# Performance work log

Hardware: AMD Instinct MI355X
Metric: run time of the kernel (lower is better)

The kernel has to match this reference:

```python
import jax, jax.numpy as jnp
import numpy as np

H = 1024
V = 50257
S = 4096

def setup_inputs() -> dict:
    key = jax.random.key(0)
    ks = jax.random.split(key, 16)
    s = 0.02
    return {
        "word_input": jax.random.randint(ks[0], (1,), 0, V),
        "h0": jax.random.normal(ks[1], (1, 1, H), jnp.float32),
        "c0": jax.random.normal(ks[2], (1, 1, H), jnp.float32),
        "encoder_outputs": jax.random.normal(ks[3], (S, 1, H), jnp.float32),
        "embedding": jax.random.normal(ks[4], (V, H), jnp.float32) * s,
        "W_ih": jax.random.normal(ks[5], (4 * H, H), jnp.float32) * s,
        "W_hh": jax.random.normal(ks[6], (4 * H, H), jnp.float32) * s,
        "b_ih": jnp.zeros((4 * H,), jnp.float32),
        "b_hh": jnp.zeros((4 * H,), jnp.float32),
        "attn_W": jax.random.normal(ks[7], (H, H), jnp.float32) * s,
        "attn_b": jnp.zeros((H,), jnp.float32),
        "out_W": jax.random.normal(ks[8], (V, 2 * H), jnp.float32) * s,
        "out_b": jnp.zeros((V,), jnp.float32),
    }


def reference(word_input, h0, c0, encoder_outputs, embedding, W_ih, W_hh,
              b_ih, b_hh, attn_W, attn_b, out_W, out_b):
    # Embedding lookup: (1, H)
    x = embedding[word_input]
    h_prev = h0[0]  # (1, H)
    c_prev = c0[0]  # (1, H)
    # Single-step single-layer LSTM (PyTorch gate order i, f, g, o)
    gates = x @ W_ih.T + b_ih + h_prev @ W_hh.T + b_hh  # (1, 4H)
    i_g, f_g, g_g, o_g = jnp.split(gates, 4, axis=1)
    c_new = jax.nn.sigmoid(f_g) * c_prev + jax.nn.sigmoid(i_g) * jnp.tanh(g_g)
    h_new = jax.nn.sigmoid(o_g) * jnp.tanh(c_new)  # (1, H) == rnn_output
    # Attention ('general'): score_i = hidden . (W_a e_i + b_a), vectorized over S
    enc = encoder_outputs[:, 0, :]  # (S, H)
    scores = (enc @ attn_W.T + attn_b) @ h_new[0]  # (S,)
    attn_w = jax.nn.softmax(scores)  # (S,)
    context = attn_w @ enc  # (H,)
    # Output projection + log_softmax
    feat = jnp.concatenate([h_new[0], context])  # (2H,)
    logits = feat @ out_W.T + out_b  # (V,)
    output = jax.nn.log_softmax(logits)[None, :]  # (1, V)
    return (output, h_new[None], c_new[None], attn_w[None, None, :])
```

## Files before the change

### kernel.cpp

```cpp
#include <hip/hip_runtime.h>
#include <math.h>

#define H 1024
#define V 50257
#define S 4096

#define OUT_H (V)
#define OUT_C (V + H)
#define OUT_A (V + 2 * H)

#define WS_LOGITS 0
#define WS_V      50260
#define WS_CTX    (WS_V + H)
#define WS_SCORES (WS_CTX + H)
#define WS_SB     (WS_SCORES + S)
#define WS_PM     (WS_SB + 4)
#define WS_PL     (WS_PM + 32)

__global__ __launch_bounds__(256) void lstm_kernel(
    const int* __restrict__ word, const float* __restrict__ emb,
    const float* __restrict__ Wih, const float* __restrict__ Whh,
    const float* __restrict__ bih, const float* __restrict__ bhh,
    const float* __restrict__ h0, const float* __restrict__ c0,
    float* __restrict__ out)
{
    int j = blockIdx.x;
    int t = threadIdx.x;
    const float4* x4 = (const float4*)(emb + (size_t)word[0] * H);
    const float4* h4 = (const float4*)h0;
    float acc[4];
#pragma unroll
    for (int r = 0; r < 4; r++) {
        int row = j + r * H;
        const float4* wi = (const float4*)(Wih + (size_t)row * H);
        const float4* wh = (const float4*)(Whh + (size_t)row * H);
        float4 a = wi[t], b = x4[t];
        float s = a.x * b.x + a.y * b.y + a.z * b.z + a.w * b.w;
        float4 c = wh[t], d = h4[t];
        s += c.x * d.x + c.y * d.y + c.z * d.z + c.w * d.w;
        acc[r] = s;
    }
    __shared__ float red[256];
    __shared__ float gates[4];
    for (int r = 0; r < 4; r++) {
        red[t] = acc[r];
        __syncthreads();
        for (int off = 128; off > 0; off >>= 1) {
            if (t < off) red[t] += red[t + off];
            __syncthreads();
        }
        if (t == 0) gates[r] = red[0];
        __syncthreads();
    }
    if (t == 0) {
        float ig = gates[0] + bih[j]         + bhh[j];
        float fg = gates[1] + bih[j + H]     + bhh[j + H];
        float gg = gates[2] + bih[j + 2 * H] + bhh[j + 2 * H];
        float og = gates[3] + bih[j + 3 * H] + bhh[j + 3 * H];
        float si = 1.f / (1.f + expf(-ig));
        float sf = 1.f / (1.f + expf(-fg));
        float so = 1.f / (1.f + expf(-og));
        float cn = sf * c0[j] + si * tanhf(gg);
        float hn = so * tanhf(cn);
        out[OUT_C + j] = cn;
        out[OUT_H + j] = hn;
    }
}

__global__ __launch_bounds__(256) void init_kernel(
    const float* __restrict__ attn_b, const float* __restrict__ out, float* __restrict__ ws)
{
    int b = blockIdx.x, t = threadIdx.x;
    if (b == 0) {
        const float* h = out + OUT_H;
        float acc = 0.f;
        for (int k = t; k < H; k += 256) acc += attn_b[k] * h[k];
        __shared__ float red[256];
        red[t] = acc; __syncthreads();
        for (int off = 128; off > 0; off >>= 1) { if (t < off) red[t] += red[t + off]; __syncthreads(); }
        if (t == 0) ws[WS_SB] = red[0];
    } else if (b <= 4) {
        ws[WS_V + (b - 1) * 256 + t] = 0.f;
    } else {
        ws[WS_CTX + (b - 5) * 256 + t] = 0.f;
    }
}

__global__ __launch_bounds__(256) void attnv_kernel(
    const float* __restrict__ attn_W, const float* __restrict__ out, float* ws)
{
    int kb = blockIdx.x;
    int jb = blockIdx.y;
    int t = threadIdx.x;
    __shared__ float hs[32];
    if (t < 32) hs[t] = out[OUT_H + jb * 32 + t];
    __syncthreads();
    float acc = 0.f;
    const float* base = attn_W + (size_t)(jb * 32) * H + kb * 256 + t;
#pragma unroll 8
    for (int jj = 0; jj < 32; jj++) acc += hs[jj] * base[(size_t)jj * H];
    atomicAdd(&ws[WS_V + kb * 256 + t], acc);
}

__global__ __launch_bounds__(256) void scores_kernel(
    const float* __restrict__ enc, float* ws)
{
    int t = threadIdx.x;
    int wave = t >> 6, lane = t & 63;
    int s = blockIdx.x * 4 + wave;
    const float4* e4 = (const float4*)(enc + (size_t)s * H);
    const float4* v4 = (const float4*)(ws + WS_V);
    float acc = 0.f;
#pragma unroll
    for (int it = 0; it < 4; it++) {
        float4 a = e4[lane + 64 * it];
        float4 b = v4[lane + 64 * it];
        acc += a.x * b.x + a.y * b.y + a.z * b.z + a.w * b.w;
    }
    for (int off = 32; off > 0; off >>= 1) acc += __shfl_xor(acc, off, 64);
    if (lane == 0) ws[WS_SCORES + s] = acc + ws[WS_SB];
}

__global__ __launch_bounds__(1024) void softmax_kernel(
    const float* __restrict__ ws, float* __restrict__ out)
{
    int t = threadIdx.x;
    float x[4];
    float m = -INFINITY;
#pragma unroll
    for (int i = 0; i < 4; i++) { x[i] = ws[WS_SCORES + t + i * 1024]; m = fmaxf(m, x[i]); }
    __shared__ float red[1024];
    __shared__ float sm, sl;
    red[t] = m; __syncthreads();
    for (int off = 512; off > 0; off >>= 1) { if (t < off) red[t] = fmaxf(red[t], red[t + off]); __syncthreads(); }
    if (t == 0) sm = red[0];
    __syncthreads();
    m = sm;
    float l = 0.f;
#pragma unroll
    for (int i = 0; i < 4; i++) { x[i] = expf(x[i] - m); l += x[i]; }
    red[t] = l; __syncthreads();
    for (int off = 512; off > 0; off >>= 1) { if (t < off) red[t] += red[t + off]; __syncthreads(); }
    if (t == 0) sl = red[0];
    __syncthreads();
    float inv = 1.f / sl;
#pragma unroll
    for (int i = 0; i < 4; i++) out[OUT_A + t + i * 1024] = x[i] * inv;
}

__global__ __launch_bounds__(256) void context_kernel(
    const float* __restrict__ enc, const float* __restrict__ out, float* ws)
{
    int kb = blockIdx.x;
    int sb = blockIdx.y;
    int t = threadIdx.x;
    const float* aw = out + OUT_A;
    float acc = 0.f;
    for (int ss = 0; ss < 64; ss++) {
        int s = sb * 64 + ss;
        acc += aw[s] * enc[(size_t)s * H + kb * 256 + t];
    }
    atomicAdd(&ws[WS_CTX + kb * 256 + t], acc);
}

__global__ __launch_bounds__(256) void logits_kernel(
    const float* __restrict__ outW, const float* __restrict__ outb,
    const float* __restrict__ out, float* ws)
{
    int t = threadIdx.x;
    __shared__ float feat[2048];
#pragma unroll
    for (int i = 0; i < 8; i++) {
        int idx = t + 256 * i;
        feat[idx] = (idx < H) ? out[OUT_H + idx] : ws[WS_CTX + idx - H];
    }
    __syncthreads();
    int wave = t >> 6, lane = t & 63;
    int r = blockIdx.x * 4 + wave;
    if (r < V) {
        const float4* w4 = (const float4*)(outW + (size_t)r * 2048);
        const float4* f4 = (const float4*)feat;
        float acc = 0.f;
#pragma unroll
        for (int it = 0; it < 8; it++) {
            float4 a = w4[lane + 64 * it];
            float4 b = f4[lane + 64 * it];
            acc += a.x * b.x + a.y * b.y + a.z * b.z + a.w * b.w;
        }
        for (int off = 32; off > 0; off >>= 1) acc += __shfl_xor(acc, off, 64);
        if (lane == 0) ws[WS_LOGITS + r] = acc + outb[r];
    }
}

__global__ __launch_bounds__(256) void lse_partial_kernel(float* ws)
{
    int t = threadIdx.x, b = blockIdx.x;
    float m = -INFINITY, l = 0.f;
    for (int i = b * 256 + t; i < V; i += 32 * 256) {
        float x = ws[WS_LOGITS + i];
        float nm = fmaxf(m, x);
        l = l * expf(m - nm) + expf(x - nm);
        m = nm;
    }
    __shared__ float sm[256], sl[256];
    sm[t] = m; sl[t] = l; __syncthreads();
    for (int off = 128; off > 0; off >>= 1) {
        if (t < off) {
            float m2 = sm[t + off], l2 = sl[t + off];
            float nm = fmaxf(sm[t], m2);
            sl[t] = sl[t] * expf(sm[t] - nm) + l2 * expf(m2 - nm);
            sm[t] = nm;
        }
        __syncthreads();
    }
    if (t == 0) { ws[WS_PM + b] = sm[0]; ws[WS_PL + b] = sl[0]; }
}

__global__ __launch_bounds__(256) void lsout_kernel(const float* __restrict__ ws, float* __restrict__ out)
{
    __shared__ float fm, fl;
    int t = threadIdx.x;
    if (t == 0) {
        float m = -INFINITY, l = 0.f;
        for (int p = 0; p < 32; p++) {
            float m2 = ws[WS_PM + p], l2 = ws[WS_PL + p];
            float nm = fmaxf(m, m2);
            l = l * expf(m - nm) + l2 * expf(m2 - nm);
            m = nm;
        }
        fm = m; fl = logf(l);
    }
    __syncthreads();
    int i = blockIdx.x * 256 + t;
    if (i < V) out[i] = ws[WS_LOGITS + i] - fm - fl;
}

extern "C" void kernel_launch(void* const* d_in, const int* in_sizes, int n_in,
                              void* d_out, int out_size, void* d_ws, size_t ws_size,
                              hipStream_t stream) {
    const int*   word   = (const int*)d_in[0];
    const float* h0     = (const float*)d_in[1];
    const float* c0     = (const float*)d_in[2];
    const float* enc    = (const float*)d_in[3];
    const float* emb    = (const float*)d_in[4];
    const float* Wih    = (const float*)d_in[5];
    const float* Whh    = (const float*)d_in[6];
    const float* bih    = (const float*)d_in[7];
    const float* bhh    = (const float*)d_in[8];
    const float* attn_W = (const float*)d_in[9];
    const float* attn_b = (const float*)d_in[10];
    const float* outW   = (const float*)d_in[11];
    const float* outb   = (const float*)d_in[12];
    float* out = (float*)d_out;
    float* ws  = (float*)d_ws;

    lstm_kernel<<<H, 256, 0, stream>>>(word, emb, Wih, Whh, bih, bhh, h0, c0, out);
    init_kernel<<<9, 256, 0, stream>>>(attn_b, out, ws);
    attnv_kernel<<<dim3(4, 32), 256, 0, stream>>>(attn_W, out, ws);
    scores_kernel<<<S / 4, 256, 0, stream>>>(enc, ws);
    softmax_kernel<<<1, 1024, 0, stream>>>(ws, out);
    context_kernel<<<dim3(4, 64), 256, 0, stream>>>(enc, out, ws);
    logits_kernel<<<(V + 3) / 4, 256, 0, stream>>>(outW, outb, out, ws);
    lse_partial_kernel<<<32, 256, 0, stream>>>(ws);
    lsout_kernel<<<(V + 255) / 256, 256, 0, stream>>>(ws, out);
}
```

Baseline: 682.2 us.

## Split output projection and overlap its h-half with attention kernels

The output GEMV is split into an h_new half and a context half. The h_new half (about 50k rows by 1024) is spread as extra blocks across the attnv, scores and context launches, filling otherwise idle GPU capacity during the small attention stages. A final kernel adds the context half. The init kernel is folded into the LSTM launch, the attention-bias dot product moves into attnv via atomics, and the LSTM reduction now uses wave shuffles instead of shared-memory trees. This reads the out_W h-half separately, and logits are now built by read-modify-write in workspace.

```diff
diff --git a/kernel.cpp b/kernel.cpp
--- a/kernel.cpp
+++ b/kernel.cpp
@@ -16,43 +16,80 @@
 #define WS_SB     (WS_SCORES + S)
 #define WS_PM     (WS_SB + 4)
 #define WS_PL     (WS_PM + 32)
+#define WS_H      (WS_PL + 32)
+
+#define GEMV_A_BLOCKS 938
+#define GEMV_S_BLOCKS 938
+#define GEMV_C_BLOCKS 1266
+#define GEMV_S_BASE 15008
+#define GEMV_C_BASE 30016
+
+__device__ __forceinline__ float wave_red(float v) {
+#pragma unroll
+    for (int off = 32; off > 0; off >>= 1) v += __shfl_xor(v, off, 64);
+    return v;
+}
+
+__device__ __forceinline__ void gemv_h_block(
+    const float* __restrict__ outW, const float* __restrict__ outb,
+    const float* __restrict__ h, float* __restrict__ ws, int base, int t)
+{
+    int wave = t >> 6, lane = t & 63;
+    const float4* h4 = (const float4*)h;
+    float4 hv0 = h4[lane], hv1 = h4[lane + 64], hv2 = h4[lane + 128], hv3 = h4[lane + 192];
+    int r0 = base + wave * 4;
+#pragma unroll
+    for (int i = 0; i < 4; i++) {
+        int r = r0 + i;
+        if (r < V) {
+            const float4* w4 = (const float4*)(outW + (size_t)r * 2048);
+            float4 a = w4[lane];
+            float acc = a.x * hv0.x + a.y * hv0.y + a.z * hv0.z + a.w * hv0.w;
+            a = w4[lane + 64];  acc += a.x * hv1.x + a.y * hv1.y + a.z * hv1.z + a.w * hv1.w;
+            a = w4[lane + 128]; acc += a.x * hv2.x + a.y * hv2.y + a.z * hv2.z + a.w * hv2.w;
+            a = w4[lane + 192]; acc += a.x * hv3.x + a.y * hv3.y + a.z * hv3.z + a.w * hv3.w;
+            acc = wave_red(acc);
+            if (lane == 0) ws[WS_LOGITS + r] = acc + outb[r];
+        }
+    }
+}
 
 __global__ __launch_bounds__(256) void lstm_kernel(
     const int* __restrict__ word, const float* __restrict__ emb,
     const float* __restrict__ Wih, const float* __restrict__ Whh,
     const float* __restrict__ bih, const float* __restrict__ bhh,
     const float* __restrict__ h0, const float* __restrict__ c0,
-    float* __restrict__ out)
-{
-    int j = blockIdx.x;
-    int t = threadIdx.x;
+    float* __restrict__ out, float* __restrict__ ws)
+{
+    int b = blockIdx.x, t = threadIdx.x;
+    if (b >= H) {
+        int z = b - H;
+        if (z < 4)      ws[WS_V + z * 256 + t] = 0.f;
+        else if (z < 8) ws[WS_CTX + (z - 4) * 256 + t] = 0.f;
+        else if (t == 0) ws[WS_SB] = 0.f;
+        return;
+    }
+    int wave = t >> 6, lane = t & 63;
+    int row = b + wave * H;
     const float4* x4 = (const float4*)(emb + (size_t)word[0] * H);
     const float4* h4 = (const float4*)h0;
-    float acc[4];
-#pragma unroll
-    for (int r = 0; r < 4; r++) {
-        int row = j + r * H;
-        const float4* wi = (const float4*)(Wih + (size_t)row * H);
-        const float4* wh = (const float4*)(Whh + (size_t)row * H);
-        float4 a = wi[t], b = x4[t];
-        float s = a.x * b.x + a.y * b.y + a.z * b.z + a.w * b.w;
-        float4 c = wh[t], d = h4[t];
-        s += c.x * d.x + c.y * d.y + c.z * d.z + c.w * d.w;
-        acc[r] = s;
-    }
-    __shared__ float red[256];
+    const float4* wi = (const float4*)(Wih + (size_t)row * H);
+    const float4* wh = (const float4*)(Whh + (size_t)row * H);
+    float acc = 0.f;
+#pragma unroll
+    for (int k = 0; k < 4; k++) {
+        int idx = lane + 64 * k;
+        float4 a = wi[idx], xb = x4[idx];
+        acc += a.x * xb.x + a.y * xb.y + a.z * xb.z + a.w * xb.w;
+        float4 c = wh[idx], hb = h4[idx];
+        acc += c.x * hb.x + c.y * hb.y + c.z * hb.z + c.w * hb.w;
+    }
+    acc = wave_red(acc);
     __shared__ float gates[4];
-    for (int r = 0; r < 4; r++) {
-        red[t] = acc[r];
-        __syncthreads();
-        for (int off = 128; off > 0; off >>= 1) {
-            if (t < off) red[t] += red[t + off];
-            __syncthreads();
-        }
-        if (t == 0) gates[r] = red[0];
-        __syncthreads();
-    }
+    if (lane == 0) gates[wave] = acc;
+    __syncthreads();
     if (t == 0) {
+        int j = b;
         float ig = gates[0] + bih[j]         + bhh[j];
         float fg = gates[1] + bih[j + H]     + bhh[j + H];
         float gg = gates[2] + bih[j + 2 * H] + bhh[j + 2 * H];
@@ -64,61 +101,59 @@
         float hn = so * tanhf(cn);
         out[OUT_C + j] = cn;
         out[OUT_H + j] = hn;
-    }
-}
-
-__global__ __launch_bounds__(256) void init_kernel(
-    const float* __restrict__ attn_b, const float* __restrict__ out, float* __restrict__ ws)
-{
-    int b = blockIdx.x, t = threadIdx.x;
-    if (b == 0) {
-        const float* h = out + OUT_H;
+        ws[WS_H + j]   = hn;
+    }
+}
+
+__global__ __launch_bounds__(256) void attnv_kernel(
+    const float* __restrict__ attn_W, const float* __restrict__ attn_b,
+    const float* __restrict__ out, const float* __restrict__ outW,
+    const float* __restrict__ outb, float* ws)
+{
+    int b = blockIdx.x, t = threadIdx.x;
+    if (b < 128) {
+        int jb = b & 31, kb = b >> 5;
+        __shared__ float hs[32];
+        if (t < 32) hs[t] = out[OUT_H + jb * 32 + t];
+        __syncthreads();
         float acc = 0.f;
-        for (int k = t; k < H; k += 256) acc += attn_b[k] * h[k];
-        __shared__ float red[256];
-        red[t] = acc; __syncthreads();
-        for (int off = 128; off > 0; off >>= 1) { if (t < off) red[t] += red[t + off]; __syncthreads(); }
-        if (t == 0) ws[WS_SB] = red[0];
-    } else if (b <= 4) {
-        ws[WS_V + (b - 1) * 256 + t] = 0.f;
+        const float* base = attn_W + (size_t)(jb * 32) * H + kb * 256 + t;
+#pragma unroll 8
+        for (int jj = 0; jj < 32; jj++) acc += hs[jj] * base[(size_t)jj * H];
+        atomicAdd(&ws[WS_V + kb * 256 + t], acc);
+        if (kb == 0 && t < 32) {
+            float p = hs[t] * attn_b[jb * 32 + t];
+#pragma unroll
+            for (int off = 16; off > 0; off >>= 1) p += __shfl_xor(p, off, 32);
+            if (t == 0) atomicAdd(&ws[WS_SB], p);
+        }
     } else {
-        ws[WS_CTX + (b - 5) * 256 + t] = 0.f;
-    }
-}
-
-__global__ __launch_bounds__(256) void attnv_kernel(
-    const float* __restrict__ attn_W, const float* __restrict__ out, float* ws)
-{
-    int kb = blockIdx.x;
-    int jb = blockIdx.y;
-    int t = threadIdx.x;
-    __shared__ float hs[32];
-    if (t < 32) hs[t] = out[OUT_H + jb * 32 + t];
-    __syncthreads();
-    float acc = 0.f;
-    const float* base = attn_W + (size_t)(jb * 32) * H + kb * 256 + t;
-#pragma unroll 8
-    for (int jj = 0; jj < 32; jj++) acc += hs[jj] * base[(size_t)jj * H];
-    atomicAdd(&ws[WS_V + kb * 256 + t], acc);
+        gemv_h_block(outW, outb, ws + WS_H, ws, (b - 128) * 16, t);
+    }
 }
 
 __global__ __launch_bounds__(256) void scores_kernel(
-    const float* __restrict__ enc, float* ws)
-{
-    int t = threadIdx.x;
-    int wave = t >> 6, lane = t & 63;
-    int s = blockIdx.x * 4 + wave;
-    const float4* e4 = (const float4*)(enc + (size_t)s * H);
-    const float4* v4 = (const float4*)(ws + WS_V);
-    float acc = 0.f;
-#pragma unroll
-    for (int it = 0; it < 4; it++) {
-        float4 a = e4[lane + 64 * it];
-        float4 b = v4[lane + 64 * it];
-        acc += a.x * b.x + a.y * b.y + a.z * b.z + a.w * b.w;
-    }
-    for (int off = 32; off > 0; off >>= 1) acc += __shfl_xor(acc, off, 64);
-    if (lane == 0) ws[WS_SCORES + s] = acc + ws[WS_SB];
+    const float* __restrict__ enc, const float* __restrict__ outW,
+    const float* __restrict__ outb, float* ws)
+{
+    int b = blockIdx.x, t = threadIdx.x;
+    int wave = t >> 6, lane = t & 63;
+    if (b < S / 4) {
+        int s = b * 4 + wave;
+        const float4* e4 = (const float4*)(enc + (size_t)s * H);
+        const float4* v4 = (const float4*)(ws + WS_V);
+        float acc = 0.f;
+#pragma unroll
+        for (int it = 0; it < 4; it++) {
+            float4 a = e4[lane + 64 * it];
+            float4 bb = v4[lane + 64 * it];
+            acc += a.x * bb.x + a.y * bb.y + a.z * bb.z + a.w * bb.w;
+        }
+        acc = wave_red(acc);
+        if (lane == 0) ws[WS_SCORES + s] = acc + ws[WS_SB];
+    } else {
+        gemv_h_block(outW, outb, ws + WS_H, ws, GEMV_S_BASE + (b - S / 4) * 16, t);
+    }
 }
 
 __global__ __launch_bounds__(1024) void softmax_kernel(
@@ -149,46 +184,45 @@
 }
 
 __global__ __launch_bounds__(256) void context_kernel(
-    const float* __restrict__ enc, const float* __restrict__ out, float* ws)
-{
-    int kb = blockIdx.x;
-    int sb = blockIdx.y;
+    const float* __restrict__ enc, const float* __restrict__ out,
+    const float* __restrict__ outW, const float* __restrict__ outb, float* ws)
+{
+    int b = blockIdx.x, t = threadIdx.x;
+    if (b < 256) {
+        int sb = b >> 2, kb = b & 3;
+        const float* aw = out + OUT_A;
+        float acc = 0.f;
+        for (int ss = 0; ss < 64; ss++) {
+            int s = sb * 64 + ss;
+            acc += aw[s] * enc[(size_t)s * H + kb * 256 + t];
+        }
+        atomicAdd(&ws[WS_CTX + kb * 256 + t], acc);
+    } else {
+        gemv_h_block(outW, outb, ws + WS_H, ws, GEMV_C_BASE + (b - 256) * 16, t);
+    }
+}
+
+__global__ __launch_bounds__(256) void logits_ctx_kernel(
+    const float* __restrict__ outW, float* ws)
+{
     int t = threadIdx.x;
-    const float* aw = out + OUT_A;
-    float acc = 0.f;
-    for (int ss = 0; ss < 64; ss++) {
-        int s = sb * 64 + ss;
-        acc += aw[s] * enc[(size_t)s * H + kb * 256 + t];
-    }
-    atomicAdd(&ws[WS_CTX + kb * 256 + t], acc);
-}
-
-__global__ __launch_bounds__(256) void logits_kernel(
-    const float* __restrict__ outW, const float* __restrict__ outb,
-    const float* __restrict__ out, float* ws)
-{
-    int t = threadIdx.x;
-    __shared__ float feat[2048];
-#pragma unroll
-    for (int i = 0; i < 8; i++) {
-        int idx = t + 256 * i;
-        feat[idx] = (idx < H) ? out[OUT_H + idx] : ws[WS_CTX + idx - H];
-    }
-    __syncthreads();
-    int wave = t >> 6, lane = t & 63;
-    int r = blockIdx.x * 4 + wave;
-    if (r < V) {
-        const float4* w4 = (const float4*)(outW + (size_t)r * 2048);
-        const float4* f4 = (const float4*)feat;
-        float acc = 0.f;
-#pragma unroll
-        for (int it = 0; it < 8; it++) {
-            float4 a = w4[lane + 64 * it];
-            float4 b = f4[lane + 64 * it];
-            acc += a.x * b.x + a.y * b.y + a.z * b.z + a.w * b.w;
-        }
-        for (int off = 32; off > 0; off >>= 1) acc += __shfl_xor(acc, off, 64);
-        if (lane == 0) ws[WS_LOGITS + r] = acc + outb[r];
+    int wave = t >> 6, lane = t & 63;
+    const float4* c4 = (const float4*)(ws + WS_CTX);
+    float4 cv0 = c4[lane], cv1 = c4[lane + 64], cv2 = c4[lane + 128], cv3 = c4[lane + 192];
+    int r0 = blockIdx.x * 16 + wave * 4;
+#pragma unroll
+    for (int i = 0; i < 4; i++) {
+        int r = r0 + i;
+        if (r < V) {
+            const float4* w4 = (const float4*)(outW + (size_t)r * 2048 + 1024);
+            float4 a = w4[lane];
+            float acc = a.x * cv0.x + a.y * cv0.y + a.z * cv0.z + a.w * cv0.w;
+            a = w4[lane + 64];  acc += a.x * cv1.x + a.y * cv1.y + a.z * cv1.z + a.w * cv1.w;
+            a = w4[lane + 128]; acc += a.x * cv2.x + a.y * cv2.y + a.z * cv2.z + a.w * cv2.w;
+            a = w4[lane + 192]; acc += a.x * cv3.x + a.y * cv3.y + a.z * cv3.z + a.w * cv3.w;
+            acc = wave_red(acc);
+            if (lane == 0) ws[WS_LOGITS + r] += acc;
+        }
     }
 }
 
@@ -254,13 +288,12 @@
     float* out = (float*)d_out;
     float* ws  = (float*)d_ws;
 
-    lstm_kernel<<<H, 256, 0, stream>>>(word, emb, Wih, Whh, bih, bhh, h0, c0, out);
-    init_kernel<<<9, 256, 0, stream>>>(attn_b, out, ws);
-    attnv_kernel<<<dim3(4, 32), 256, 0, stream>>>(attn_W, out, ws);
-    scores_kernel<<<S / 4, 256, 0, stream>>>(enc, ws);
+    lstm_kernel<<<H + 9, 256, 0, stream>>>(word, emb, Wih, Whh, bih, bhh, h0, c0, out, ws);
+    attnv_kernel<<<128 + GEMV_A_BLOCKS, 256, 0, stream>>>(attn_W, attn_b, out, outW, outb, ws);
+    scores_kernel<<<S / 4 + GEMV_S_BLOCKS, 256, 0, stream>>>(enc, outW, outb, ws);
     softmax_kernel<<<1, 1024, 0, stream>>>(ws, out);
-    context_kernel<<<dim3(4, 64), 256, 0, stream>>>(enc, out, ws);
-    logits_kernel<<<(V + 3) / 4, 256, 0, stream>>>(outW, outb, out, ws);
+    context_kernel<<<256 + GEMV_C_BLOCKS, 256, 0, stream>>>(enc, out, outW, outb, ws);
+    logits_ctx_kernel<<<(V + 15) / 16, 256, 0, stream>>>(outW, ws);
     lse_partial_kernel<<<32, 256, 0, stream>>>(ws);
     lsout_kernel<<<(V + 255) / 256, 256, 0, stream>>>(ws, out);
 }
```

Result: no change. 675.5 us (-1.0%).
